# Performance work log

Hardware: AMD Instinct MI355X
Metric: run time of the kernel (lower is better)

## Reference

```python
import jax, jax.numpy as jnp
import numpy as np

K_DIM = 768
HEADS = 8
HEAD_DIM = K_DIM // HEADS  # 96


def setup_inputs() -> dict:
    key = jax.random.key(0)
    ks = jax.random.split(key, 6)
    b, t = 4, 2048
    scale = 1.0 / np.sqrt(HEAD_DIM)
    return {
        "input_x": jax.random.normal(ks[0], (b, t, K_DIM), dtype=jnp.float32),
        "Wq": jax.random.normal(ks[1], (HEAD_DIM, HEAD_DIM), dtype=jnp.float32) * scale,
        "Wk": jax.random.normal(ks[2], (HEAD_DIM, HEAD_DIM), dtype=jnp.float32) * scale,
        "Wv": jax.random.normal(ks[3], (HEAD_DIM, HEAD_DIM), dtype=jnp.float32) * scale,
        "Wu": jax.random.normal(ks[4], (K_DIM, K_DIM), dtype=jnp.float32) * (1.0 / np.sqrt(K_DIM)),
        "bu": jax.random.normal(ks[5], (K_DIM,), dtype=jnp.float32) * 0.01,
    }


def reference(input_x, Wq, Wk, Wv, Wu, bu):
    b, t, k = input_x.shape
    h, d = HEADS, k // HEADS
    # split into heads: [b, t, h, d]; per-head projections share the same d x d weights
    x = input_x.reshape(b, t, h, d)
    inv4 = 1.0 / (k ** 0.25)
    q = jnp.einsum("bthd,od->btho", x, Wq) * inv4  # scaled queries
    kk = jnp.einsum("bthd,od->btho", x, Wk) * inv4  # scaled keys
    v = jnp.einsum("bthd,od->btho", x, Wv)
    # full attention matrix [b, h, t, t] (materialized, as in the original bmm impl)
    scores = jnp.einsum("bthd,bshd->bhts", q, kk)
    attn = jax.nn.softmax(scores, axis=-1)
    out = jnp.einsum("bhts,bshd->bthd", attn, v).reshape(b, t, k)
    return out @ Wu.T + bu
```

## Files before the change

kernel.cpp:

```cpp
#include <hip/hip_runtime.h>
#include <hip/hip_bf16.h>
#include <math.h>

#define TB 2048
#define NB 4
#define NH 8
#define HD 96
#define KD 768

typedef unsigned short u16;
typedef __attribute__((ext_vector_type(4))) u16 u16x4;
typedef __attribute__((ext_vector_type(8))) u16 u16x8;
typedef __attribute__((ext_vector_type(4))) float f32x4;
typedef __attribute__((ext_vector_type(8))) __bf16 bf16x8;

__device__ __forceinline__ u16 f2bf(float f) {
    unsigned u = __builtin_bit_cast(unsigned, f);
    u += 0x7FFFu + ((u >> 16) & 1u);
    return (u16)(u >> 16);
}
__device__ __forceinline__ bf16x8 cast8(u16x8 u) { return __builtin_bit_cast(bf16x8, u); }

__global__ __launch_bounds__(256) void qkv_proj(
    const float* __restrict__ x, const float* __restrict__ Wq,
    const float* __restrict__ Wk, const float* __restrict__ Wv,
    u16* __restrict__ Q, u16* __restrict__ Kout, u16* __restrict__ VT, float inv4)
{
    __shared__ __align__(16) u16 Wl[3][96][104];
    const int tid = threadIdx.x;
    for (int idx = tid; idx < 3 * 9216; idx += 256) {
        int m = idx / 9216, rem = idx % 9216;
        const float* Wsrc = (m == 0) ? Wq : (m == 1) ? Wk : Wv;
        float scale = (m < 2) ? inv4 : 1.0f;
        int r = rem / 96, c = rem % 96;
        Wl[m][r][c] = f2bf(Wsrc[rem] * scale);
    }
    __syncthreads();

    const int w = tid >> 6, l = tid & 63;
    const int lc = l & 15, lk = l >> 4;
    const int bh = blockIdx.y, b = bh >> 3, h = bh & 7;
    const int t0 = blockIdx.x * 64 + w * 16;

    bf16x8 afrag[3];
    {
        const float* xp = x + ((long)((b * TB + t0 + lc) * NH + h)) * HD + 8 * lk;
#pragma unroll
        for (int c = 0; c < 3; ++c) {
            f32x4 f0 = *(const f32x4*)(xp + c * 32);
            f32x4 f1 = *(const f32x4*)(xp + c * 32 + 4);
            u16x8 u;
#pragma unroll
            for (int j = 0; j < 4; ++j) { u[j] = f2bf(f0[j]); u[4 + j] = f2bf(f1[j]); }
            afrag[c] = cast8(u);
        }
    }

    const f32x4 Z4 = {0.f, 0.f, 0.f, 0.f};
    u16* outs[2] = {Q, Kout};
#pragma unroll
    for (int m = 0; m < 2; ++m) {
        f32x4 acc[6];
#pragma unroll
        for (int nt = 0; nt < 6; ++nt) acc[nt] = Z4;
#pragma unroll
        for (int c = 0; c < 3; ++c) {
#pragma unroll
            for (int nt = 0; nt < 6; ++nt) {
                u16x8 bw = *(const u16x8*)&Wl[m][nt * 16 + lc][c * 32 + 8 * lk];
                acc[nt] = __builtin_amdgcn_mfma_f32_16x16x32_bf16(afrag[c], cast8(bw), acc[nt], 0, 0, 0);
            }
        }
#pragma unroll
        for (int reg = 0; reg < 4; ++reg) {
            int t = t0 + lk * 4 + reg;
            u16* op = outs[m] + ((long)bh * TB + t) * HD;
#pragma unroll
            for (int nt = 0; nt < 6; ++nt)
                op[nt * 16 + lc] = f2bf(acc[nt][reg]);
        }
    }
    {
        f32x4 acc[6];
#pragma unroll
        for (int nt = 0; nt < 6; ++nt) acc[nt] = Z4;
#pragma unroll
        for (int c = 0; c < 3; ++c) {
#pragma unroll
            for (int nt = 0; nt < 6; ++nt) {
                u16x8 aw = *(const u16x8*)&Wl[2][nt * 16 + lc][c * 32 + 8 * lk];
                acc[nt] = __builtin_amdgcn_mfma_f32_16x16x32_bf16(cast8(aw), afrag[c], acc[nt], 0, 0, 0);
            }
        }
#pragma unroll
        for (int nt = 0; nt < 6; ++nt)
#pragma unroll
            for (int reg = 0; reg < 4; ++reg) {
                int o = nt * 16 + lk * 4 + reg;
                VT[((long)bh * HD + o) * TB + t0 + lc] = f2bf(acc[nt][reg]);
            }
    }
}

__global__ __launch_bounds__(512) void attn(
    const u16* __restrict__ Q, const u16* __restrict__ Kin, const u16* __restrict__ VT,
    u16* __restrict__ O)
{
    __shared__ __align__(16) u16 Kl[64][104];
    __shared__ __align__(16) u16 Vt[96][72];
    __shared__ __align__(16) u16 Pl[8][16][72];

    const int tid = threadIdx.x;
    const int w = tid >> 6, l = tid & 63;
    const int lc = l & 15, lk = l >> 4;
    const int bh = blockIdx.y;
    const int q0 = blockIdx.x * 128 + w * 16;

    const u16* Qb = Q + (long)bh * TB * HD;
    const u16* Kb = Kin + (long)bh * TB * HD;
    const u16* Vb = VT + (long)bh * HD * TB;

    const u16* gbase[3]; u16* lptr[3]; int mult[3];
#pragma unroll
    for (int ci = 0; ci < 3; ++ci) {
        int ch = tid + ci * 512;
        if (ch < 768) {
            int row = ch / 12, cc = (ch % 12) * 8;
            gbase[ci] = Kb + row * HD + cc;
            mult[ci] = HD;
            lptr[ci] = &Kl[row][cc];
        } else {
            int c2 = ch - 768;
            int d = c2 >> 3, sc = (c2 & 7) * 8;
            gbase[ci] = Vb + (long)d * TB + sc;
            mult[ci] = 1;
            lptr[ci] = &Vt[d][sc];
        }
    }

    bf16x8 aq[3];
#pragma unroll
    for (int c = 0; c < 3; ++c)
        aq[c] = cast8(*(const u16x8*)(Qb + (long)(q0 + lc) * HD + c * 32 + 8 * lk));

    u16x8 r[3];
#pragma unroll
    for (int ci = 0; ci < 3; ++ci) r[ci] = *(const u16x8*)(gbase[ci]);

    float m_st = -1e30f, l_st = 0.f;
    f32x4 accO[6];
    const f32x4 Z4 = {0.f, 0.f, 0.f, 0.f};
#pragma unroll
    for (int nt = 0; nt < 6; ++nt) accO[nt] = Z4;

    for (int st = 0; st < TB / 64; ++st) {
        __syncthreads();
#pragma unroll
        for (int ci = 0; ci < 3; ++ci) *(u16x8*)lptr[ci] = r[ci];
        int s1 = (st + 1) * 64; if (s1 > TB - 64) s1 = TB - 64;
#pragma unroll
        for (int ci = 0; ci < 3; ++ci) r[ci] = *(const u16x8*)(gbase[ci] + (long)s1 * mult[ci]);
        __syncthreads();

        f32x4 s[4];
#pragma unroll
        for (int nt = 0; nt < 4; ++nt) s[nt] = Z4;
#pragma unroll
        for (int c = 0; c < 3; ++c) {
#pragma unroll
            for (int nt = 0; nt < 4; ++nt) {
                u16x8 kf = *(const u16x8*)&Kl[nt * 16 + lc][c * 32 + 8 * lk];
                s[nt] = __builtin_amdgcn_mfma_f32_16x16x32_bf16(cast8(kf), aq[c], s[nt], 0, 0, 0);
            }
        }
        float tm = -1e30f;
#pragma unroll
        for (int nt = 0; nt < 4; ++nt)
#pragma unroll
            for (int reg = 0; reg < 4; ++reg) tm = fmaxf(tm, s[nt][reg]);
        tm = fmaxf(tm, __shfl_xor(tm, 16));
        tm = fmaxf(tm, __shfl_xor(tm, 32));
        float mnew = fmaxf(m_st, tm);
        float alpha = __expf(m_st - mnew);
        m_st = mnew;
        float p[4][4]; float sum = 0.f;
#pragma unroll
        for (int nt = 0; nt < 4; ++nt)
#pragma unroll
            for (int reg = 0; reg < 4; ++reg) {
                float pv = __expf(s[nt][reg] - mnew);
                p[nt][reg] = pv;
                sum += pv;
            }
        sum += __shfl_xor(sum, 16);
        sum += __shfl_xor(sum, 32);
        l_st = l_st * alpha + sum;

#pragma unroll
        for (int nt = 0; nt < 4; ++nt) {
            u16x4 pk = { f2bf(p[nt][0]), f2bf(p[nt][1]), f2bf(p[nt][2]), f2bf(p[nt][3]) };
            *(u16x4*)&Pl[w][lc][nt * 16 + lk * 4] = pk;
        }
        float ar[4];
#pragma unroll
        for (int reg = 0; reg < 4; ++reg) ar[reg] = __shfl(alpha, lk * 4 + reg, 16);
#pragma unroll
        for (int nt = 0; nt < 6; ++nt)
#pragma unroll
            for (int reg = 0; reg < 4; ++reg) accO[nt][reg] *= ar[reg];
        asm volatile("s_waitcnt lgkmcnt(0)" ::: "memory");

#pragma unroll
        for (int c2 = 0; c2 < 2; ++c2) {
            bf16x8 pa = cast8(*(const u16x8*)&Pl[w][lc][c2 * 32 + 8 * lk]);
#pragma unroll
            for (int nt = 0; nt < 6; ++nt) {
                u16x8 bv = *(const u16x8*)&Vt[nt * 16 + lc][c2 * 32 + 8 * lk];
                accO[nt] = __builtin_amdgcn_mfma_f32_16x16x32_bf16(pa, cast8(bv), accO[nt], 0, 0, 0);
            }
        }
    }

    const int b = bh >> 3, h = bh & 7;
    float linv[4];
#pragma unroll
    for (int reg = 0; reg < 4; ++reg) linv[reg] = 1.0f / __shfl(l_st, lk * 4 + reg, 16);
#pragma unroll
    for (int reg = 0; reg < 4; ++reg) {
        int t = q0 + lk * 4 + reg;
        u16* op = O + ((long)(b * TB + t)) * KD + h * HD;
#pragma unroll
        for (int nt = 0; nt < 6; ++nt)
            op[nt * 16 + lc] = f2bf(accO[nt][reg] * linv[reg]);
    }
}

__global__ __launch_bounds__(256) void out_gemm(
    const u16* __restrict__ O, const float* __restrict__ Wu,
    const float* __restrict__ bu, float* __restrict__ out)
{
    __shared__ __align__(16) u16 Al[64][40];
    __shared__ __align__(16) u16 Bl[128][40];
    const int tid = threadIdx.x;
    const int w = tid >> 6, l = tid & 63;
    const int lc = l & 15, lk = l >> 4;
    const int m0 = blockIdx.x * 64, n0 = blockIdx.y * 128;

    f32x4 acc[8];
    const f32x4 Z4 = {0.f, 0.f, 0.f, 0.f};
#pragma unroll
    for (int nt = 0; nt < 8; ++nt) acc[nt] = Z4;

    for (int c0 = 0; c0 < KD; c0 += 32) {
        __syncthreads();
        {
            int row = tid >> 2, cc = (tid & 3) * 8;
            *(u16x8*)&Al[row][cc] = *(const u16x8*)(O + (long)(m0 + row) * KD + c0 + cc);
        }
        {
            int row = tid >> 1, cc = (tid & 1) * 16;
            const float* src = Wu + (long)(n0 + row) * KD + c0 + cc;
            f32x4 f0 = *(const f32x4*)(src);
            f32x4 f1 = *(const f32x4*)(src + 4);
            f32x4 f2 = *(const f32x4*)(src + 8);
            f32x4 f3 = *(const f32x4*)(src + 12);
            u16x8 u0, u1;
#pragma unroll
            for (int j = 0; j < 4; ++j) {
                u0[j] = f2bf(f0[j]); u0[4 + j] = f2bf(f1[j]);
                u1[j] = f2bf(f2[j]); u1[4 + j] = f2bf(f3[j]);
            }
            *(u16x8*)&Bl[row][cc] = u0;
            *(u16x8*)&Bl[row][cc + 8] = u1;
        }
        __syncthreads();

        bf16x8 a = cast8(*(const u16x8*)&Al[w * 16 + lc][8 * lk]);
#pragma unroll
        for (int nt = 0; nt < 8; ++nt) {
            u16x8 bb = *(const u16x8*)&Bl[nt * 16 + lc][8 * lk];
            acc[nt] = __builtin_amdgcn_mfma_f32_16x16x32_bf16(a, cast8(bb), acc[nt], 0, 0, 0);
        }
    }

#pragma unroll
    for (int reg = 0; reg < 4; ++reg) {
        int rr = m0 + w * 16 + lk * 4 + reg;
        float* op = out + (long)rr * KD + n0;
#pragma unroll
        for (int nt = 0; nt < 8; ++nt)
            op[nt * 16 + lc] = acc[nt][reg] + bu[n0 + nt * 16 + lc];
    }
}

extern "C" void kernel_launch(void* const* d_in, const int* in_sizes, int n_in,
                              void* d_out, int out_size, void* d_ws, size_t ws_size,
                              hipStream_t stream) {
    const float* x  = (const float*)d_in[0];
    const float* Wq = (const float*)d_in[1];
    const float* Wk = (const float*)d_in[2];
    const float* Wv = (const float*)d_in[3];
    const float* Wu = (const float*)d_in[4];
    const float* bu = (const float*)d_in[5];
    float* out = (float*)d_out;

    u16* ws = (u16*)d_ws;
    const size_t SZ = (size_t)NB * NH * TB * HD;
    u16* Q  = ws;
    u16* Kq = ws + SZ;
    u16* VT = ws + 2 * SZ;
    u16* O  = ws + 3 * SZ;

    const float inv4 = 1.0f / powf((float)KD, 0.25f);

    qkv_proj<<<dim3(TB / 64, NB * NH), dim3(256), 0, stream>>>(x, Wq, Wk, Wv, Q, Kq, VT, inv4);
    attn<<<dim3(TB / 128, NB * NH), dim3(512), 0, stream>>>(Q, Kq, VT, O);
    out_gemm<<<dim3((NB * TB) / 64, KD / 128), dim3(256), 0, stream>>>(O, Wu, bu, out);
}
```

Before: 227.4 us.

## Use 32x32 MFMA tiles in attention with register-resident P and lazy rescale

The attention kernel moves from 16x16x32 to 32x32x16 bf16 MFMA tiles, with 32 queries per wave and 256 per block. The probability tile stays in registers, repacked via packed bf16 converts and cross-half shuffles, so the LDS round trip for P goes away. Rescaling of the running max is skipped unless it grows by more than 8, and the output is written with vectorized stores. Wu is converted to bf16 once in a separate kernel into the Q workspace region, which is dead after attention, and the out GEMM prefetches its tiles in registers. The cost is fewer blocks in the attention grid and higher register pressure.

After: 199.3 us. -12.4%, faster.

```diff
diff --git a/kernel.cpp b/kernel.cpp
--- a/kernel.cpp
+++ b/kernel.cpp
@@ -12,6 +12,8 @@
 typedef __attribute__((ext_vector_type(4))) u16 u16x4;
 typedef __attribute__((ext_vector_type(8))) u16 u16x8;
 typedef __attribute__((ext_vector_type(4))) float f32x4;
+typedef __attribute__((ext_vector_type(16))) float f32x16;
+typedef __attribute__((ext_vector_type(4))) unsigned u32x4;
 typedef __attribute__((ext_vector_type(8))) __bf16 bf16x8;
 
 __device__ __forceinline__ u16 f2bf(float f) {
@@ -20,6 +22,11 @@
     return (u16)(u >> 16);
 }
 __device__ __forceinline__ bf16x8 cast8(u16x8 u) { return __builtin_bit_cast(bf16x8, u); }
+__device__ __forceinline__ unsigned pkbf(float a, float b) {
+    unsigned w;
+    asm("v_cvt_pk_bf16_f32 %0, %1, %2" : "=v"(w) : "v"(a), "v"(b));
+    return w;
+}
 
 __global__ __launch_bounds__(256) void qkv_proj(
     const float* __restrict__ x, const float* __restrict__ Wq,
@@ -108,13 +115,12 @@
 {
     __shared__ __align__(16) u16 Kl[64][104];
     __shared__ __align__(16) u16 Vt[96][72];
-    __shared__ __align__(16) u16 Pl[8][16][72];
 
     const int tid = threadIdx.x;
     const int w = tid >> 6, l = tid & 63;
-    const int lc = l & 15, lk = l >> 4;
+    const int m32 = l & 31, hi = l >> 5;
     const int bh = blockIdx.y;
-    const int q0 = blockIdx.x * 128 + w * 16;
+    const int q0 = blockIdx.x * 256 + w * 32;
 
     const u16* Qb = Q + (long)bh * TB * HD;
     const u16* Kb = Kin + (long)bh * TB * HD;
@@ -138,20 +144,21 @@
         }
     }
 
-    bf16x8 aq[3];
-#pragma unroll
-    for (int c = 0; c < 3; ++c)
-        aq[c] = cast8(*(const u16x8*)(Qb + (long)(q0 + lc) * HD + c * 32 + 8 * lk));
+    bf16x8 qb[6];
+#pragma unroll
+    for (int kk = 0; kk < 6; ++kk)
+        qb[kk] = cast8(*(const u16x8*)(Qb + (long)(q0 + m32) * HD + kk * 16 + 8 * hi));
 
     u16x8 r[3];
 #pragma unroll
     for (int ci = 0; ci < 3; ++ci) r[ci] = *(const u16x8*)(gbase[ci]);
 
     float m_st = -1e30f, l_st = 0.f;
-    f32x4 accO[6];
-    const f32x4 Z4 = {0.f, 0.f, 0.f, 0.f};
-#pragma unroll
-    for (int nt = 0; nt < 6; ++nt) accO[nt] = Z4;
+    f32x16 accO[3];
+#pragma unroll
+    for (int dt = 0; dt < 3; ++dt)
+#pragma unroll
+        for (int rr = 0; rr < 16; ++rr) accO[dt][rr] = 0.f;
 
     for (int st = 0; st < TB / 64; ++st) {
         __syncthreads();
@@ -162,81 +169,100 @@
         for (int ci = 0; ci < 3; ++ci) r[ci] = *(const u16x8*)(gbase[ci] + (long)s1 * mult[ci]);
         __syncthreads();
 
-        f32x4 s[4];
-#pragma unroll
-        for (int nt = 0; nt < 4; ++nt) s[nt] = Z4;
-#pragma unroll
-        for (int c = 0; c < 3; ++c) {
-#pragma unroll
-            for (int nt = 0; nt < 4; ++nt) {
-                u16x8 kf = *(const u16x8*)&Kl[nt * 16 + lc][c * 32 + 8 * lk];
-                s[nt] = __builtin_amdgcn_mfma_f32_16x16x32_bf16(cast8(kf), aq[c], s[nt], 0, 0, 0);
-            }
-        }
-        float tm = -1e30f;
-#pragma unroll
-        for (int nt = 0; nt < 4; ++nt)
-#pragma unroll
-            for (int reg = 0; reg < 4; ++reg) tm = fmaxf(tm, s[nt][reg]);
-        tm = fmaxf(tm, __shfl_xor(tm, 16));
+        f32x16 sa[2];
+#pragma unroll
+        for (int st2 = 0; st2 < 2; ++st2) {
+#pragma unroll
+            for (int rr = 0; rr < 16; ++rr) sa[st2][rr] = 0.f;
+#pragma unroll
+            for (int kk = 0; kk < 6; ++kk) {
+                u16x8 kf = *(const u16x8*)&Kl[st2 * 32 + m32][kk * 16 + 8 * hi];
+                sa[st2] = __builtin_amdgcn_mfma_f32_32x32x16_bf16(cast8(kf), qb[kk], sa[st2], 0, 0, 0);
+            }
+        }
+
+        float tm = sa[0][0];
+#pragma unroll
+        for (int st2 = 0; st2 < 2; ++st2)
+#pragma unroll
+            for (int rr = 0; rr < 16; ++rr) tm = fmaxf(tm, sa[st2][rr]);
         tm = fmaxf(tm, __shfl_xor(tm, 32));
-        float mnew = fmaxf(m_st, tm);
-        float alpha = __expf(m_st - mnew);
-        m_st = mnew;
-        float p[4][4]; float sum = 0.f;
-#pragma unroll
-        for (int nt = 0; nt < 4; ++nt)
-#pragma unroll
-            for (int reg = 0; reg < 4; ++reg) {
-                float pv = __expf(s[nt][reg] - mnew);
-                p[nt][reg] = pv;
+        if (!__all(tm - m_st <= 8.0f)) {
+            float mnew = fmaxf(m_st, tm);
+            float alpha = __expf(m_st - mnew);
+#pragma unroll
+            for (int dt = 0; dt < 3; ++dt)
+#pragma unroll
+                for (int rr = 0; rr < 16; ++rr) accO[dt][rr] *= alpha;
+            l_st *= alpha;
+            m_st = mnew;
+        }
+        float sum = 0.f;
+#pragma unroll
+        for (int st2 = 0; st2 < 2; ++st2)
+#pragma unroll
+            for (int rr = 0; rr < 16; ++rr) {
+                float pv = __expf(sa[st2][rr] - m_st);
+                sa[st2][rr] = pv;
                 sum += pv;
             }
-        sum += __shfl_xor(sum, 16);
         sum += __shfl_xor(sum, 32);
-        l_st = l_st * alpha + sum;
-
-#pragma unroll
-        for (int nt = 0; nt < 4; ++nt) {
-            u16x4 pk = { f2bf(p[nt][0]), f2bf(p[nt][1]), f2bf(p[nt][2]), f2bf(p[nt][3]) };
-            *(u16x4*)&Pl[w][lc][nt * 16 + lk * 4] = pk;
-        }
-        float ar[4];
-#pragma unroll
-        for (int reg = 0; reg < 4; ++reg) ar[reg] = __shfl(alpha, lk * 4 + reg, 16);
-#pragma unroll
-        for (int nt = 0; nt < 6; ++nt)
-#pragma unroll
-            for (int reg = 0; reg < 4; ++reg) accO[nt][reg] *= ar[reg];
-        asm volatile("s_waitcnt lgkmcnt(0)" ::: "memory");
-
-#pragma unroll
-        for (int c2 = 0; c2 < 2; ++c2) {
-            bf16x8 pa = cast8(*(const u16x8*)&Pl[w][lc][c2 * 32 + 8 * lk]);
-#pragma unroll
-            for (int nt = 0; nt < 6; ++nt) {
-                u16x8 bv = *(const u16x8*)&Vt[nt * 16 + lc][c2 * 32 + 8 * lk];
-                accO[nt] = __builtin_amdgcn_mfma_f32_16x16x32_bf16(pa, cast8(bv), accO[nt], 0, 0, 0);
+        l_st += sum;
+
+#pragma unroll
+        for (int st2 = 0; st2 < 2; ++st2) {
+            unsigned A1 = pkbf(sa[st2][0], sa[st2][1]);
+            unsigned A2 = pkbf(sa[st2][2], sa[st2][3]);
+            unsigned B1 = pkbf(sa[st2][4], sa[st2][5]);
+            unsigned B2 = pkbf(sa[st2][6], sa[st2][7]);
+            unsigned A3 = pkbf(sa[st2][8], sa[st2][9]);
+            unsigned A4 = pkbf(sa[st2][10], sa[st2][11]);
+            unsigned B3 = pkbf(sa[st2][12], sa[st2][13]);
+            unsigned B4 = pkbf(sa[st2][14], sa[st2][15]);
+            unsigned xA1 = __shfl_xor((int)A1, 32), xA2 = __shfl_xor((int)A2, 32);
+            unsigned xB1 = __shfl_xor((int)B1, 32), xB2 = __shfl_xor((int)B2, 32);
+            unsigned xA3 = __shfl_xor((int)A3, 32), xA4 = __shfl_xor((int)A4, 32);
+            unsigned xB3 = __shfl_xor((int)B3, 32), xB4 = __shfl_xor((int)B4, 32);
+            u32x4 t0 = { hi ? xB1 : A1, hi ? xB2 : A2, hi ? B1 : xA1, hi ? B2 : xA2 };
+            u32x4 t1 = { hi ? xB3 : A3, hi ? xB4 : A4, hi ? B3 : xA3, hi ? B4 : xA4 };
+            bf16x8 pb0 = __builtin_bit_cast(bf16x8, t0);
+            bf16x8 pb1 = __builtin_bit_cast(bf16x8, t1);
+#pragma unroll
+            for (int dt = 0; dt < 3; ++dt) {
+                u16x8 vfa = *(const u16x8*)&Vt[dt * 32 + m32][st2 * 32 + 8 * hi];
+                accO[dt] = __builtin_amdgcn_mfma_f32_32x32x16_bf16(cast8(vfa), pb0, accO[dt], 0, 0, 0);
+            }
+#pragma unroll
+            for (int dt = 0; dt < 3; ++dt) {
+                u16x8 vfb = *(const u16x8*)&Vt[dt * 32 + m32][st2 * 32 + 16 + 8 * hi];
+                accO[dt] = __builtin_amdgcn_mfma_f32_32x32x16_bf16(cast8(vfb), pb1, accO[dt], 0, 0, 0);
             }
         }
     }
 
     const int b = bh >> 3, h = bh & 7;
-    float linv[4];
-#pragma unroll
-    for (int reg = 0; reg < 4; ++reg) linv[reg] = 1.0f / __shfl(l_st, lk * 4 + reg, 16);
-#pragma unroll
-    for (int reg = 0; reg < 4; ++reg) {
-        int t = q0 + lk * 4 + reg;
-        u16* op = O + ((long)(b * TB + t)) * KD + h * HD;
-#pragma unroll
-        for (int nt = 0; nt < 6; ++nt)
-            op[nt * 16 + lc] = f2bf(accO[nt][reg] * linv[reg]);
-    }
+    float linv = 1.0f / l_st;
+    int t = q0 + m32;
+    u16* op = O + ((long)(b * TB + t)) * KD + h * HD;
+#pragma unroll
+    for (int dt = 0; dt < 3; ++dt)
+#pragma unroll
+        for (int q4 = 0; q4 < 4; ++q4) {
+            u16x4 v = { f2bf(accO[dt][q4 * 4 + 0] * linv), f2bf(accO[dt][q4 * 4 + 1] * linv),
+                        f2bf(accO[dt][q4 * 4 + 2] * linv), f2bf(accO[dt][q4 * 4 + 3] * linv) };
+            *(u16x4*)(op + dt * 32 + q4 * 8 + 4 * hi) = v;
+        }
+}
+
+__global__ __launch_bounds__(256) void wu_conv(const float* __restrict__ Wu, u16* __restrict__ Wub) {
+    int i = (blockIdx.x * 256 + threadIdx.x) * 4;
+    f32x4 f = *(const f32x4*)(Wu + i);
+    u16x4 o = { f2bf(f[0]), f2bf(f[1]), f2bf(f[2]), f2bf(f[3]) };
+    *(u16x4*)(Wub + i) = o;
 }
 
 __global__ __launch_bounds__(256) void out_gemm(
-    const u16* __restrict__ O, const float* __restrict__ Wu,
+    const u16* __restrict__ O, const u16* __restrict__ Wub,
     const float* __restrict__ bu, float* __restrict__ out)
 {
     __shared__ __align__(16) u16 Al[64][40];
@@ -246,33 +272,28 @@
     const int lc = l & 15, lk = l >> 4;
     const int m0 = blockIdx.x * 64, n0 = blockIdx.y * 128;
 
+    const int arow = tid >> 2, acc_ = (tid & 3) * 8;
+    const int brow0 = tid >> 2, bcc0 = (tid & 3) * 8;
+    const int brow1 = (tid + 256) >> 2, bcc1 = (tid & 3) * 8;
+
     f32x4 acc[8];
     const f32x4 Z4 = {0.f, 0.f, 0.f, 0.f};
 #pragma unroll
     for (int nt = 0; nt < 8; ++nt) acc[nt] = Z4;
 
+    u16x8 ra = *(const u16x8*)(O + (long)(m0 + arow) * KD + acc_);
+    u16x8 rb0 = *(const u16x8*)(Wub + (long)(n0 + brow0) * KD + bcc0);
+    u16x8 rb1 = *(const u16x8*)(Wub + (long)(n0 + brow1) * KD + bcc1);
+
     for (int c0 = 0; c0 < KD; c0 += 32) {
         __syncthreads();
-        {
-            int row = tid >> 2, cc = (tid & 3) * 8;
-            *(u16x8*)&Al[row][cc] = *(const u16x8*)(O + (long)(m0 + row) * KD + c0 + cc);
-        }
-        {
-            int row = tid >> 1, cc = (tid & 1) * 16;
-            const float* src = Wu + (long)(n0 + row) * KD + c0 + cc;
-            f32x4 f0 = *(const f32x4*)(src);
-            f32x4 f1 = *(const f32x4*)(src + 4);
-            f32x4 f2 = *(const f32x4*)(src + 8);
-            f32x4 f3 = *(const f32x4*)(src + 12);
-            u16x8 u0, u1;
-#pragma unroll
-            for (int j = 0; j < 4; ++j) {
-                u0[j] = f2bf(f0[j]); u0[4 + j] = f2bf(f1[j]);
-                u1[j] = f2bf(f2[j]); u1[4 + j] = f2bf(f3[j]);
-            }
-            *(u16x8*)&Bl[row][cc] = u0;
-            *(u16x8*)&Bl[row][cc + 8] = u1;
-        }
+        *(u16x8*)&Al[arow][acc_] = ra;
+        *(u16x8*)&Bl[brow0][bcc0] = rb0;
+        *(u16x8*)&Bl[brow1][bcc1] = rb1;
+        int cn = c0 + 32; if (cn > KD - 32) cn = KD - 32;
+        ra = *(const u16x8*)(O + (long)(m0 + arow) * KD + cn + acc_);
+        rb0 = *(const u16x8*)(Wub + (long)(n0 + brow0) * KD + cn + bcc0);
+        rb1 = *(const u16x8*)(Wub + (long)(n0 + brow1) * KD + cn + bcc1);
         __syncthreads();
 
         bf16x8 a = cast8(*(const u16x8*)&Al[w * 16 + lc][8 * lk]);
@@ -306,14 +327,16 @@
 
     u16* ws = (u16*)d_ws;
     const size_t SZ = (size_t)NB * NH * TB * HD;
-    u16* Q  = ws;
-    u16* Kq = ws + SZ;
-    u16* VT = ws + 2 * SZ;
-    u16* O  = ws + 3 * SZ;
+    u16* Q   = ws;
+    u16* Kq  = ws + SZ;
+    u16* VT  = ws + 2 * SZ;
+    u16* O   = ws + 3 * SZ;
+    u16* Wub = ws;
 
     const float inv4 = 1.0f / powf((float)KD, 0.25f);
 
     qkv_proj<<<dim3(TB / 64, NB * NH), dim3(256), 0, stream>>>(x, Wq, Wk, Wv, Q, Kq, VT, inv4);
-    attn<<<dim3(TB / 128, NB * NH), dim3(512), 0, stream>>>(Q, Kq, VT, O);
-    out_gemm<<<dim3((NB * TB) / 64, KD / 128), dim3(256), 0, stream>>>(O, Wu, bu, out);
-}
+    attn<<<dim3(TB / 256, NB * NH), dim3(512), 0, stream>>>(Q, Kq, VT, O);
+    wu_conv<<<dim3((KD * KD) / 1024), dim3(256), 0, stream>>>(Wu, Wub);
+    out_gemm<<<dim3((NB * TB) / 64, KD / 128), dim3(256), 0, stream>>>(O, Wub, bu, out);
+}
```
